# Performance work log

Hardware: AMD Instinct MI355X
Metric: run time of the kernel (lower is better)

The kernel has to match this reference:

```python
import jax, jax.numpy as jnp
import numpy as np

H = 96
W = 96
FX = 96.0
FY = 96.0
NEAR = 0.3
EPS = 1e-8


def q2r(quat):
    # quat: [N,4] (w,x,y,z) -> [N,3,3]
    q = quat / (jnp.linalg.norm(quat, axis=-1, keepdims=True) + 1e-12)
    w, x, y, z = q[:, 0], q[:, 1], q[:, 2], q[:, 3]
    R = jnp.stack([
        1 - 2 * (y * y + z * z), 2 * (x * y - w * z), 2 * (x * z + w * y),
        2 * (x * y + w * z), 1 - 2 * (x * x + z * z), 2 * (y * z - w * x),
        2 * (x * z - w * y), 2 * (y * z + w * x), 1 - 2 * (x * x + y * y),
    ], axis=-1).reshape(-1, 3, 3)
    return R


def setup_inputs() -> dict:
    key = jax.random.key(0)
    ks = jax.random.split(key, 8)
    N = 4096
    pos_xy = jax.random.uniform(ks[0], (N, 2), minval=-2.0, maxval=2.0, dtype=jnp.float32)
    pos_z = jax.random.uniform(ks[1], (N, 1), minval=2.0, maxval=6.0, dtype=jnp.float32)
    pos = jnp.concatenate([pos_xy, pos_z], axis=-1)
    rgb = jax.random.normal(ks[2], (N, 3), dtype=jnp.float32)
    opa = jax.random.normal(ks[3], (N,), dtype=jnp.float32)
    quat = jax.random.normal(ks[4], (N, 4), dtype=jnp.float32)
    scale = jax.random.uniform(ks[5], (N, 3), dtype=jnp.float32) * 0.05 + 0.005
    rot = jnp.eye(3, dtype=jnp.float32)
    tran = jnp.zeros(3, dtype=jnp.float32)
    return {"pos": pos, "rgb": rgb, "opa": opa, "quat": quat, "scale": scale, "rot": rot, "tran": tran}


def reference(pos, rgb, opa, quat, scale, rot, tran):
    # ---- project: world -> camera -> image space ----
    cam = pos @ rot.T + tran[None, :]              # [N,3]
    x, y, z = cam[:, 0], cam[:, 1], cam[:, 2]
    r = jnp.linalg.norm(cam, axis=-1)              # depth = ray length (camera_to_image)
    mean2d = jnp.stack([x / z, y / z], axis=-1)    # [N,2]

    # jacobian of (x/z, y/z, |p|) wrt camera-space point, [N,3,3]
    zeros = jnp.zeros_like(z)
    J = jnp.stack([
        1.0 / z, zeros, -x / (z * z),
        zeros, 1.0 / z, -y / (z * z),
        x / r, y / r, z / r,
    ], axis=-1).reshape(-1, 3, 3)

    # ---- 3D covariance: R S S^T R^T ----
    R = q2r(quat)                                   # [N,3,3]
    s = jnp.abs(scale) + 1e-4                       # [N,3]
    RS = R * s[:, None, :]                          # R @ diag(s)
    cov3d = jnp.einsum('nij,nkj->nik', RS, RS)      # [N,3,3]

    # ---- 2D covariance: (J W) cov3d (J W)^T, upper-left 2x2 ----
    JW = jnp.einsum('nij,jk->nik', J, rot)          # [N,3,3]
    cov2d = jnp.einsum('nij,njk,nlk->nil', JW, cov3d, JW)[:, :2, :2]  # [N,2,2]

    a = cov2d[:, 0, 0] + EPS
    d = cov2d[:, 1, 1] + EPS
    b = 0.5 * (cov2d[:, 0, 1] + cov2d[:, 1, 0])
    det = a * d - b * b
    inv_a = d / det
    inv_b = -b / det
    inv_d = a / det

    rgb_act = jax.nn.sigmoid(rgb)                   # [N,3]
    opa_act = jax.nn.sigmoid(opa)                   # [N]

    # ---- per-pixel gaussian evaluation in normalized image space ----
    u = (jnp.arange(W, dtype=jnp.float32) + 0.5 - W / 2) / FX   # [W]
    v = (jnp.arange(H, dtype=jnp.float32) + 0.5 - H / 2) / FY   # [H]
    pu = jnp.tile(u, H)                                          # [P]
    pv = jnp.repeat(v, W)                                        # [P]

    dx = pu[None, :] - mean2d[:, 0:1]               # [N,P]
    dy = pv[None, :] - mean2d[:, 1:2]               # [N,P]
    power = -0.5 * (inv_a[:, None] * dx * dx + 2.0 * inv_b[:, None] * dx * dy + inv_d[:, None] * dy * dy)
    alpha = opa_act[:, None] * jnp.exp(power)       # [N,P]
    alpha = jnp.clip(alpha, 0.0, 0.99)
    valid = (z > NEAR).astype(alpha.dtype)[:, None]
    alpha = alpha * valid

    # ---- depth-sorted alpha compositing ----
    order = jnp.argsort(r)                          # near -> far
    alpha_s = alpha[order]                          # [N,P]
    rgb_s = rgb_act[order]                          # [N,3]

    log_1m = jnp.log1p(-alpha_s)                    # [N,P]
    cum = jnp.cumsum(log_1m, axis=0)
    logT = jnp.concatenate([jnp.zeros((1, alpha_s.shape[1]), alpha_s.dtype), cum[:-1]], axis=0)
    w = jnp.exp(logT) * alpha_s                     # [N,P] blending weights
    img = jnp.einsum('np,nc->pc', w, rgb_s)         # [P,3]
    return img.reshape(H, W, 3)
```

## Files before the change

kernel.cpp:

```cpp
#include <hip/hip_runtime.h>
#include <math.h>

#define N_G   4096
#define IMW   96
#define TILE  6
#define TILES_X 16
#define NTILE (TILES_X*TILES_X)
#define NTHR  1024
#define NW    (NTHR/64)
#define NST   (N_G/NTHR)
#define NPX   (TILE*TILE)
#define NSEG  16
#define BCAP  2048
#define CAP   512
#define FXI   (1.0f/96.0f)
#define NEARP 0.3f
#define EPSV  1e-8f
#define LOG2E 1.4426950408889634f
#define LN2   0.6931471805599453f
#define CULL_K 26.0f

typedef unsigned long long ull;
typedef __attribute__((ext_vector_type(2))) unsigned long long ull2;

__global__ __launch_bounds__(NTHR, 1) void splat_k(
    const float* __restrict__ pos, const float* __restrict__ rgb,
    const float* __restrict__ opa, const float* __restrict__ quat,
    const float* __restrict__ scale, const float* __restrict__ rot,
    const float* __restrict__ tran, float* __restrict__ out)
{
    __shared__ unsigned int bl[BCAP];
    __shared__ __align__(16) ull skey[CAP+2];
    __shared__ int sslot[CAP];
    __shared__ float4 g0[CAP], g1[CAP];
    __shared__ float  g2[CAP];
    __shared__ float4 pix[NSEG*NPX];
    __shared__ int psum[4][CAP];
    __shared__ int bcnt_sh, cnt_sh;

    const int t = threadIdx.x;
    const int tile = blockIdx.x;
    const int tx = tile % TILES_X, ty = tile / TILES_X;
    const float u0 = ((float)(tx*TILE) + 0.5f - 48.0f) * FXI;
    const float u1 = u0 + (TILE-1) * FXI;
    const float v0 = ((float)(ty*TILE) + 0.5f - 48.0f) * FXI;
    const float v1 = v0 + (TILE-1) * FXI;
    const int wid = t >> 6, lane = t & 63;

    if (t == 0) { bcnt_sh = 0; cnt_sh = 0; }

    float R00=rot[0],R01=rot[1],R02=rot[2];
    float R10=rot[3],R11=rot[4],R12=rot[5];
    float R20=rot[6],R21=rot[7],R22=rot[8];
    float t0=tran[0], t1=tran[1], t2=tran[2];

    float pp0[NST], pp1[NST], pp2[NST], po[NST], ps0[NST], ps1[NST], ps2[NST];
    #pragma unroll
    for (int st = 0; st < NST; st++) {
        int gi = st*NTHR + t;
        pp0[st]=pos[gi*3+0]; pp1[st]=pos[gi*3+1]; pp2[st]=pos[gi*3+2];
        po[st]=opa[gi];
        ps0[st]=scale[gi*3+0]; ps1[st]=scale[gi*3+1]; ps2[st]=scale[gi*3+2];
    }
    __syncthreads();

    #pragma unroll
    for (int st = 0; st < NST; st++) {
        int gi = st*NTHR + t;
        float x = R00*pp0[st] + R01*pp1[st] + R02*pp2[st] + t0;
        float y = R10*pp0[st] + R11*pp1[st] + R12*pp2[st] + t1;
        float z = R20*pp0[st] + R21*pp1[st] + R22*pp2[st] + t2;
        float invz = 1.0f/z;
        float mu = x*invz, mv = y*invz;

        float inz2 = invz*invz;
        float fn = 2.0f*inz2 + (x*x + y*y)*inz2*inz2;
        float smax = fmaxf(fmaxf(fabsf(ps0[st]), fabsf(ps1[st])), fabsf(ps2[st])) + 1e-4f;
        float lmax = fn*smax*smax + EPSV;
        float amp = CULL_K + 1.0f + fminf(0.0f, po[st]*LOG2E);
        float r2b = amp * lmax * (2.0f*LN2) * 1.02f;

        float cu = fminf(fmaxf(mu, u0), u1);
        float cv = fminf(fmaxf(mv, v0), v1);
        float ddx = mu - cu, ddy = mv - cv;
        bool flag = (z > NEARP) && (amp > 0.0f) && (ddx*ddx + ddy*ddy <= r2b);

        ull m = __ballot(flag);
        int nm = __popcll(m);
        int base = 0;
        if (lane == 0 && nm) base = atomicAdd(&bcnt_sh, nm);
        base = __shfl(base, 0);
        if (flag) {
            int p = base + __popcll(m & ((1ull << lane) - 1ull));
            if (p < BCAP) bl[p] = (unsigned int)gi;
        }
    }
    __syncthreads();
    int bcnt = bcnt_sh; if (bcnt > BCAP) bcnt = BCAP;

    for (int s0i = 0; s0i < bcnt; s0i += NTHR) {
        int s = s0i + t;
        bool flag = false;
        float4 o0, o1; float ocb = 0.0f, rr = 0.0f;
        unsigned int gi = 0;
        if (s < bcnt) {
            gi = bl[s];
            float p0=pos[gi*3+0], p1=pos[gi*3+1], p2=pos[gi*3+2];
            float x = R00*p0 + R01*p1 + R02*p2 + t0;
            float y = R10*p0 + R11*p1 + R12*p2 + t1;
            float z = R20*p0 + R21*p1 + R22*p2 + t2;
            rr = sqrtf(x*x + y*y + z*z);
            float invz = 1.0f/z;
            float mu = x*invz, mv = y*invz;

            float J02 = -x*invz*invz, J12 = -y*invz*invz;
            float JW00 = invz*R00 + J02*R20;
            float JW01 = invz*R01 + J02*R21;
            float JW02 = invz*R02 + J02*R22;
            float JW10 = invz*R10 + J12*R20;
            float JW11 = invz*R11 + J12*R21;
            float JW12 = invz*R12 + J12*R22;

            float qw=quat[gi*4+0], qx=quat[gi*4+1], qy=quat[gi*4+2], qz=quat[gi*4+3];
            float qn = sqrtf(qw*qw+qx*qx+qy*qy+qz*qz) + 1e-12f;
            float qi = 1.0f/qn;
            qw*=qi; qx*=qi; qy*=qi; qz*=qi;
            float Q00=1.f-2.f*(qy*qy+qz*qz), Q01=2.f*(qx*qy-qw*qz), Q02=2.f*(qx*qz+qw*qy);
            float Q10=2.f*(qx*qy+qw*qz), Q11=1.f-2.f*(qx*qx+qz*qz), Q12=2.f*(qy*qz-qw*qx);
            float Q20=2.f*(qx*qz-qw*qy), Q21=2.f*(qy*qz+qw*qx), Q22=1.f-2.f*(qx*qx+qy*qy);

            float sa=fabsf(scale[gi*3+0])+1e-4f;
            float sb=fabsf(scale[gi*3+1])+1e-4f;
            float sc=fabsf(scale[gi*3+2])+1e-4f;
            float A00=Q00*sa,A01=Q01*sb,A02=Q02*sc;
            float A10=Q10*sa,A11=Q11*sb,A12=Q12*sc;
            float A20=Q20*sa,A21=Q21*sb,A22=Q22*sc;
            float C00=A00*A00+A01*A01+A02*A02;
            float C01=A00*A10+A01*A11+A02*A12;
            float C02=A00*A20+A01*A21+A02*A22;
            float C11=A10*A10+A11*A11+A12*A12;
            float C12=A10*A20+A11*A21+A12*A22;
            float C22=A20*A20+A21*A21+A22*A22;
            float M00=JW00*C00+JW01*C01+JW02*C02;
            float M01=JW00*C01+JW01*C11+JW02*C12;
            float M02=JW00*C02+JW01*C12+JW02*C22;
            float M10=JW10*C00+JW11*C01+JW12*C02;
            float M11=JW10*C01+JW11*C11+JW12*C12;
            float M12=JW10*C02+JW11*C12+JW12*C22;
            float a  = M00*JW00+M01*JW01+M02*JW02 + EPSV;
            float d  = M10*JW10+M11*JW11+M12*JW12 + EPSV;
            float bb = 0.5f*((M00*JW10+M01*JW11+M02*JW12)+(M10*JW00+M11*JW01+M12*JW02));
            float invdet = 1.0f/(a*d - bb*bb);
            float iaP = -0.5f*d*invdet*LOG2E;
            float ibP =  bb*invdet*LOG2E;
            float idP = -0.5f*a*invdet*LOG2E;

            float sig_o = 1.0f/(1.0f+__expf(-opa[gi]));
            float opa_eff = (z > NEARP) ? sig_o : 0.0f;

            float q00 = -iaP, q01 = -0.5f*ibP, q11 = -idP;
            float detQ = q00*q11 - q01*q01;
            float K = CULL_K + log2f(opa_eff);

            float cu = fminf(fmaxf(mu, u0), u1);
            float cv = fminf(fmaxf(mv, v0), v1);
            float ddx = mu - cu, ddy = mv - cv;
            flag = (ddx*ddx*detQ <= K*q11) && (ddy*ddy*detQ <= K*q00);

            if (flag) {
                float c0 = 1.0f/(1.0f+__expf(-rgb[gi*3+0]));
                float c1 = 1.0f/(1.0f+__expf(-rgb[gi*3+1]));
                float c2 = 1.0f/(1.0f+__expf(-rgb[gi*3+2]));
                o0 = make_float4(mu, mv, iaP, ibP);
                o1 = make_float4(idP, opa_eff, c0, c1);
                ocb = c2;
            }
        }
        ull m = __ballot(flag);
        int nm = __popcll(m);
        int base = 0;
        if (lane == 0 && nm) base = atomicAdd(&cnt_sh, nm);
        base = __shfl(base, 0);
        if (flag) {
            int p = base + __popcll(m & ((1ull << lane) - 1ull));
            if (p < CAP) {
                g0[p] = o0; g1[p] = o1; g2[p] = ocb;
                skey[p] = ((ull)__float_as_uint(rr) << 32) | gi;
            }
        }
    }
    __syncthreads();
    int cnt = cnt_sh; if (cnt > CAP) cnt = CAP;

    if (t == 0 && (cnt & 1)) skey[cnt] = ~0ull;
    __syncthreads();
    int cnt2 = cnt + (cnt & 1);
    int nq = cnt2 >> 1;
    const ull2* sk2 = (const ull2*)skey;
    const int g = t >> 8, e = t & 255;
    const bool h1 = (e < cnt), h2 = (e + 256 < cnt);
    ull kv1 = 0, kv2 = 0;
    if (h1) {
        kv1 = skey[e];
        if (h2) kv2 = skey[e + 256];
        int wA = (nq * g) >> 2;
        int wB = (nq * (g+1)) >> 2;
        int c1 = 0, c2 = 0;
        for (int w = wA; w < wB; w++) {
            ull2 p = sk2[w];
            c1 += (p.x < kv1) ? 1 : 0;
            c1 += (p.y < kv1) ? 1 : 0;
            c2 += (p.x < kv2) ? 1 : 0;
            c2 += (p.y < kv2) ? 1 : 0;
        }
        psum[g][e] = c1;
        if (h2) psum[g][e + 256] = c2;
    }
    __syncthreads();
    if (t < 256 && h1) {
        int r1 = psum[0][e] + psum[1][e] + psum[2][e] + psum[3][e];
        skey[r1]  = kv1;
        sslot[r1] = e;
        if (h2) {
            int e2 = e + 256;
            int r2 = psum[0][e2] + psum[1][e2] + psum[2][e2] + psum[3][e2];
            skey[r2]  = kv2;
            sslot[r2] = e2;
        }
    }
    __syncthreads();

    {
        const int seg = wid;
        const bool act = (lane < NPX);
        const int pid = act ? lane : 0;
        const int px = tx*TILE + (pid % TILE);
        const int py = ty*TILE + (pid / TILE);
        const float pu = ((float)px + 0.5f - 48.0f) * FXI;
        const float pv = ((float)py + 0.5f - 48.0f) * FXI;

        const int per = (cnt + NSEG - 1) / NSEG;
        const int sA = min(seg * per, cnt);
        const int sB = min(sA + per, cnt);

        float T = 1.0f, cr = 0.0f, cg = 0.0f, cb = 0.0f;
        for (int s = sA; s < sB; s++) {
            int slot = sslot[s];
            float4 a0 = g0[slot];
            float4 a1 = g1[slot];
            float  a2 = g2[slot];
            float dx = pu - a0.x;
            float dy = pv - a0.y;
            float pw = dx*(a0.z*dx + a0.w*dy) + a1.x*dy*dy;
            float al = fminf(a1.y * __builtin_amdgcn_exp2f(pw), 0.99f);
            float w = T * al;
            cr += w * a1.z;
            cg += w * a1.w;
            cb += w * a2;
            T *= (1.0f - al);
        }
        if (act) pix[seg*NPX + pid] = make_float4(cr, cg, cb, T);
    }
    __syncthreads();

    if (t < NPX) {
        float orr = 0.0f, og = 0.0f, ob = 0.0f, T2 = 1.0f;
        #pragma unroll
        for (int s = 0; s < NSEG; s++) {
            float4 P = pix[s*NPX + t];
            orr += T2 * P.x;
            og  += T2 * P.y;
            ob  += T2 * P.z;
            T2  *= P.w;
        }
        int px = tx*TILE + (t % TILE);
        int py = ty*TILE + (t / TILE);
        int pixel = py * IMW + px;
        out[pixel*3+0] = orr;
        out[pixel*3+1] = og;
        out[pixel*3+2] = ob;
    }
}

extern "C" void kernel_launch(void* const* d_in, const int* in_sizes, int n_in,
                              void* d_out, int out_size, void* d_ws, size_t ws_size,
                              hipStream_t stream) {
    const float* pos   = (const float*)d_in[0];
    const float* rgb   = (const float*)d_in[1];
    const float* opa   = (const float*)d_in[2];
    const float* quat  = (const float*)d_in[3];
    const float* scale = (const float*)d_in[4];
    const float* rot   = (const float*)d_in[5];
    const float* tran  = (const float*)d_in[6];
    float* out = (float*)d_out;

    splat_k<<<NTILE, NTHR, 0, stream>>>(pos, rgb, opa, quat, scale, rot, tran, out);
}
```

Baseline: 14.02 us.

## Split per-Gaussian preprocessing into a separate kernel shared by all tiles

Per-Gaussian projection, 2D covariance, inverse, activations and the elliptical cull extents are now computed once in a small prep kernel and written to workspace. The render kernel then does a single cull pass per tile against those precomputed extents and gathers the packed attributes. Before, every one of the 256 tiles recomputed the coarse cull for all 4096 Gaussians and the full covariance for the survivors. The cost is an extra kernel launch and global-memory round trips through the workspace, plus an exact ellipse-extent test that replaces the two-stage cull.

```diff
diff --git a/kernel.cpp b/kernel.cpp
--- a/kernel.cpp
+++ b/kernel.cpp
@@ -8,35 +8,116 @@
 #define NTILE (TILES_X*TILES_X)
 #define NTHR  1024
 #define NW    (NTHR/64)
-#define NST   (N_G/NTHR)
 #define NPX   (TILE*TILE)
 #define NSEG  16
-#define BCAP  2048
 #define CAP   512
 #define FXI   (1.0f/96.0f)
 #define NEARP 0.3f
 #define EPSV  1e-8f
 #define LOG2E 1.4426950408889634f
-#define LN2   0.6931471805599453f
 #define CULL_K 26.0f
 
 typedef unsigned long long ull;
 typedef __attribute__((ext_vector_type(2))) unsigned long long ull2;
 
-__global__ __launch_bounds__(NTHR, 1) void splat_k(
+__global__ __launch_bounds__(128) void prep_k(
     const float* __restrict__ pos, const float* __restrict__ rgb,
     const float* __restrict__ opa, const float* __restrict__ quat,
     const float* __restrict__ scale, const float* __restrict__ rot,
-    const float* __restrict__ tran, float* __restrict__ out)
+    const float* __restrict__ tran,
+    float4* __restrict__ cull, float4* __restrict__ p0a,
+    float4* __restrict__ p1a, float2* __restrict__ p2a)
 {
-    __shared__ unsigned int bl[BCAP];
+    int i = blockIdx.x * blockDim.x + threadIdx.x;
+    if (i >= N_G) return;
+
+    float R00=rot[0],R01=rot[1],R02=rot[2];
+    float R10=rot[3],R11=rot[4],R12=rot[5];
+    float R20=rot[6],R21=rot[7],R22=rot[8];
+    float t0=tran[0], t1=tran[1], t2=tran[2];
+
+    float p0 = pos[i*3+0], p1 = pos[i*3+1], p2 = pos[i*3+2];
+    float x = R00*p0 + R01*p1 + R02*p2 + t0;
+    float y = R10*p0 + R11*p1 + R12*p2 + t1;
+    float z = R20*p0 + R21*p1 + R22*p2 + t2;
+    float rr = sqrtf(x*x + y*y + z*z);
+    float invz = 1.0f/z;
+    float mu = x*invz, mv = y*invz;
+
+    float J02 = -x*invz*invz, J12 = -y*invz*invz;
+    float JW00 = invz*R00 + J02*R20;
+    float JW01 = invz*R01 + J02*R21;
+    float JW02 = invz*R02 + J02*R22;
+    float JW10 = invz*R10 + J12*R20;
+    float JW11 = invz*R11 + J12*R21;
+    float JW12 = invz*R12 + J12*R22;
+
+    float qw=quat[i*4+0], qx=quat[i*4+1], qy=quat[i*4+2], qz=quat[i*4+3];
+    float qn = sqrtf(qw*qw+qx*qx+qy*qy+qz*qz) + 1e-12f;
+    float qi = 1.0f/qn;
+    qw*=qi; qx*=qi; qy*=qi; qz*=qi;
+    float Q00=1.f-2.f*(qy*qy+qz*qz), Q01=2.f*(qx*qy-qw*qz), Q02=2.f*(qx*qz+qw*qy);
+    float Q10=2.f*(qx*qy+qw*qz), Q11=1.f-2.f*(qx*qx+qz*qz), Q12=2.f*(qy*qz-qw*qx);
+    float Q20=2.f*(qx*qz-qw*qy), Q21=2.f*(qy*qz+qw*qx), Q22=1.f-2.f*(qx*qx+qy*qy);
+
+    float sa=fabsf(scale[i*3+0])+1e-4f;
+    float sb=fabsf(scale[i*3+1])+1e-4f;
+    float sc=fabsf(scale[i*3+2])+1e-4f;
+    float A00=Q00*sa,A01=Q01*sb,A02=Q02*sc;
+    float A10=Q10*sa,A11=Q11*sb,A12=Q12*sc;
+    float A20=Q20*sa,A21=Q21*sb,A22=Q22*sc;
+    float C00=A00*A00+A01*A01+A02*A02;
+    float C01=A00*A10+A01*A11+A02*A12;
+    float C02=A00*A20+A01*A21+A02*A22;
+    float C11=A10*A10+A11*A11+A12*A12;
+    float C12=A10*A20+A11*A21+A12*A22;
+    float C22=A20*A20+A21*A21+A22*A22;
+    float M00=JW00*C00+JW01*C01+JW02*C02;
+    float M01=JW00*C01+JW01*C11+JW02*C12;
+    float M02=JW00*C02+JW01*C12+JW02*C22;
+    float M10=JW10*C00+JW11*C01+JW12*C02;
+    float M11=JW10*C01+JW11*C11+JW12*C12;
+    float M12=JW10*C02+JW11*C12+JW12*C22;
+    float a  = M00*JW00+M01*JW01+M02*JW02 + EPSV;
+    float d  = M10*JW10+M11*JW11+M12*JW12 + EPSV;
+    float bb = 0.5f*((M00*JW10+M01*JW11+M02*JW12)+(M10*JW00+M11*JW01+M12*JW02));
+    float invdet = 1.0f/(a*d - bb*bb);
+    float iaP = -0.5f*d*invdet*LOG2E;
+    float ibP =  bb*invdet*LOG2E;
+    float idP = -0.5f*a*invdet*LOG2E;
+
+    float sig_o = 1.0f/(1.0f+__expf(-opa[i]));
+    float opa_eff = (z > NEARP) ? sig_o : 0.0f;
+    float c0 = 1.0f/(1.0f+__expf(-rgb[i*3+0]));
+    float c1 = 1.0f/(1.0f+__expf(-rgb[i*3+1]));
+    float c2 = 1.0f/(1.0f+__expf(-rgb[i*3+2]));
+
+    float q00 = -iaP, q01 = -0.5f*ibP, q11 = -idP;
+    float detQ = q00*q11 - q01*q01;
+    float K = CULL_K + log2f(opa_eff);
+    float eu2, ev2;
+    if (detQ > 0.0f && K > 0.0f)      { eu2 = K*q11/detQ; ev2 = K*q00/detQ; }
+    else if (K > 0.0f)                { eu2 = 1e30f; ev2 = 1e30f; }
+    else                              { eu2 = -1.0f; ev2 = -1.0f; }
+
+    cull[i] = make_float4(mu, mv, eu2, ev2);
+    p0a[i]  = make_float4(mu, mv, iaP, ibP);
+    p1a[i]  = make_float4(idP, opa_eff, c0, c1);
+    p2a[i]  = make_float2(c2, rr);
+}
+
+__global__ __launch_bounds__(NTHR, 1) void render_k(
+    const float4* __restrict__ cull, const float4* __restrict__ p0a,
+    const float4* __restrict__ p1a, const float2* __restrict__ p2a,
+    float* __restrict__ out)
+{
     __shared__ __align__(16) ull skey[CAP+2];
     __shared__ int sslot[CAP];
     __shared__ float4 g0[CAP], g1[CAP];
     __shared__ float  g2[CAP];
     __shared__ float4 pix[NSEG*NPX];
     __shared__ int psum[4][CAP];
-    __shared__ int bcnt_sh, cnt_sh;
+    __shared__ int cnt_sh;
 
     const int t = threadIdx.x;
     const int tile = blockIdx.x;
@@ -47,135 +128,18 @@
     const float v1 = v0 + (TILE-1) * FXI;
     const int wid = t >> 6, lane = t & 63;
 
-    if (t == 0) { bcnt_sh = 0; cnt_sh = 0; }
-
-    float R00=rot[0],R01=rot[1],R02=rot[2];
-    float R10=rot[3],R11=rot[4],R12=rot[5];
-    float R20=rot[6],R21=rot[7],R22=rot[8];
-    float t0=tran[0], t1=tran[1], t2=tran[2];
-
-    float pp0[NST], pp1[NST], pp2[NST], po[NST], ps0[NST], ps1[NST], ps2[NST];
+    if (t == 0) cnt_sh = 0;
+    __syncthreads();
+
     #pragma unroll
-    for (int st = 0; st < NST; st++) {
-        int gi = st*NTHR + t;
-        pp0[st]=pos[gi*3+0]; pp1[st]=pos[gi*3+1]; pp2[st]=pos[gi*3+2];
-        po[st]=opa[gi];
-        ps0[st]=scale[gi*3+0]; ps1[st]=scale[gi*3+1]; ps2[st]=scale[gi*3+2];
-    }
-    __syncthreads();
-
-    #pragma unroll
-    for (int st = 0; st < NST; st++) {
-        int gi = st*NTHR + t;
-        float x = R00*pp0[st] + R01*pp1[st] + R02*pp2[st] + t0;
-        float y = R10*pp0[st] + R11*pp1[st] + R12*pp2[st] + t1;
-        float z = R20*pp0[st] + R21*pp1[st] + R22*pp2[st] + t2;
-        float invz = 1.0f/z;
-        float mu = x*invz, mv = y*invz;
-
-        float inz2 = invz*invz;
-        float fn = 2.0f*inz2 + (x*x + y*y)*inz2*inz2;
-        float smax = fmaxf(fmaxf(fabsf(ps0[st]), fabsf(ps1[st])), fabsf(ps2[st])) + 1e-4f;
-        float lmax = fn*smax*smax + EPSV;
-        float amp = CULL_K + 1.0f + fminf(0.0f, po[st]*LOG2E);
-        float r2b = amp * lmax * (2.0f*LN2) * 1.02f;
-
-        float cu = fminf(fmaxf(mu, u0), u1);
-        float cv = fminf(fmaxf(mv, v0), v1);
-        float ddx = mu - cu, ddy = mv - cv;
-        bool flag = (z > NEARP) && (amp > 0.0f) && (ddx*ddx + ddy*ddy <= r2b);
-
-        ull m = __ballot(flag);
-        int nm = __popcll(m);
-        int base = 0;
-        if (lane == 0 && nm) base = atomicAdd(&bcnt_sh, nm);
-        base = __shfl(base, 0);
-        if (flag) {
-            int p = base + __popcll(m & ((1ull << lane) - 1ull));
-            if (p < BCAP) bl[p] = (unsigned int)gi;
-        }
-    }
-    __syncthreads();
-    int bcnt = bcnt_sh; if (bcnt > BCAP) bcnt = BCAP;
-
-    for (int s0i = 0; s0i < bcnt; s0i += NTHR) {
-        int s = s0i + t;
-        bool flag = false;
-        float4 o0, o1; float ocb = 0.0f, rr = 0.0f;
-        unsigned int gi = 0;
-        if (s < bcnt) {
-            gi = bl[s];
-            float p0=pos[gi*3+0], p1=pos[gi*3+1], p2=pos[gi*3+2];
-            float x = R00*p0 + R01*p1 + R02*p2 + t0;
-            float y = R10*p0 + R11*p1 + R12*p2 + t1;
-            float z = R20*p0 + R21*p1 + R22*p2 + t2;
-            rr = sqrtf(x*x + y*y + z*z);
-            float invz = 1.0f/z;
-            float mu = x*invz, mv = y*invz;
-
-            float J02 = -x*invz*invz, J12 = -y*invz*invz;
-            float JW00 = invz*R00 + J02*R20;
-            float JW01 = invz*R01 + J02*R21;
-            float JW02 = invz*R02 + J02*R22;
-            float JW10 = invz*R10 + J12*R20;
-            float JW11 = invz*R11 + J12*R21;
-            float JW12 = invz*R12 + J12*R22;
-
-            float qw=quat[gi*4+0], qx=quat[gi*4+1], qy=quat[gi*4+2], qz=quat[gi*4+3];
-            float qn = sqrtf(qw*qw+qx*qx+qy*qy+qz*qz) + 1e-12f;
-            float qi = 1.0f/qn;
-            qw*=qi; qx*=qi; qy*=qi; qz*=qi;
-            float Q00=1.f-2.f*(qy*qy+qz*qz), Q01=2.f*(qx*qy-qw*qz), Q02=2.f*(qx*qz+qw*qy);
-            float Q10=2.f*(qx*qy+qw*qz), Q11=1.f-2.f*(qx*qx+qz*qz), Q12=2.f*(qy*qz-qw*qx);
-            float Q20=2.f*(qx*qz-qw*qy), Q21=2.f*(qy*qz+qw*qx), Q22=1.f-2.f*(qx*qx+qy*qy);
-
-            float sa=fabsf(scale[gi*3+0])+1e-4f;
-            float sb=fabsf(scale[gi*3+1])+1e-4f;
-            float sc=fabsf(scale[gi*3+2])+1e-4f;
-            float A00=Q00*sa,A01=Q01*sb,A02=Q02*sc;
-            float A10=Q10*sa,A11=Q11*sb,A12=Q12*sc;
-            float A20=Q20*sa,A21=Q21*sb,A22=Q22*sc;
-            float C00=A00*A00+A01*A01+A02*A02;
-            float C01=A00*A10+A01*A11+A02*A12;
-            float C02=A00*A20+A01*A21+A02*A22;
-            float C11=A10*A10+A11*A11+A12*A12;
-            float C12=A10*A20+A11*A21+A12*A22;
-            float C22=A20*A20+A21*A21+A22*A22;
-            float M00=JW00*C00+JW01*C01+JW02*C02;
-            float M01=JW00*C01+JW01*C11+JW02*C12;
-            float M02=JW00*C02+JW01*C12+JW02*C22;
-            float M10=JW10*C00+JW11*C01+JW12*C02;
-            float M11=JW10*C01+JW11*C11+JW12*C12;
-            float M12=JW10*C02+JW11*C12+JW12*C22;
-            float a  = M00*JW00+M01*JW01+M02*JW02 + EPSV;
-            float d  = M10*JW10+M11*JW11+M12*JW12 + EPSV;
-            float bb = 0.5f*((M00*JW10+M01*JW11+M02*JW12)+(M10*JW00+M11*JW01+M12*JW02));
-            float invdet = 1.0f/(a*d - bb*bb);
-            float iaP = -0.5f*d*invdet*LOG2E;
-            float ibP =  bb*invdet*LOG2E;
-            float idP = -0.5f*a*invdet*LOG2E;
-
-            float sig_o = 1.0f/(1.0f+__expf(-opa[gi]));
-            float opa_eff = (z > NEARP) ? sig_o : 0.0f;
-
-            float q00 = -iaP, q01 = -0.5f*ibP, q11 = -idP;
-            float detQ = q00*q11 - q01*q01;
-            float K = CULL_K + log2f(opa_eff);
-
-            float cu = fminf(fmaxf(mu, u0), u1);
-            float cv = fminf(fmaxf(mv, v0), v1);
-            float ddx = mu - cu, ddy = mv - cv;
-            flag = (ddx*ddx*detQ <= K*q11) && (ddy*ddy*detQ <= K*q00);
-
-            if (flag) {
-                float c0 = 1.0f/(1.0f+__expf(-rgb[gi*3+0]));
-                float c1 = 1.0f/(1.0f+__expf(-rgb[gi*3+1]));
-                float c2 = 1.0f/(1.0f+__expf(-rgb[gi*3+2]));
-                o0 = make_float4(mu, mv, iaP, ibP);
-                o1 = make_float4(idP, opa_eff, c0, c1);
-                ocb = c2;
-            }
-        }
+    for (int k = 0; k < N_G/NTHR; k++) {
+        int gi = k*NTHR + t;
+        float4 cq = cull[gi];
+        float cu = fminf(fmaxf(cq.x, u0), u1);
+        float cv = fminf(fmaxf(cq.y, v0), v1);
+        float ddx = cq.x - cu, ddy = cq.y - cv;
+        bool flag = (ddx*ddx <= cq.z) && (ddy*ddy <= cq.w);
+
         ull m = __ballot(flag);
         int nm = __popcll(m);
         int base = 0;
@@ -184,8 +148,11 @@
         if (flag) {
             int p = base + __popcll(m & ((1ull << lane) - 1ull));
             if (p < CAP) {
-                g0[p] = o0; g1[p] = o1; g2[p] = ocb;
-                skey[p] = ((ull)__float_as_uint(rr) << 32) | gi;
+                float4 a0 = p0a[gi];
+                float4 a1 = p1a[gi];
+                float2 a2 = p2a[gi];
+                g0[p] = a0; g1[p] = a1; g2[p] = a2.x;
+                skey[p] = ((ull)__float_as_uint(a2.y) << 32) | (unsigned int)gi;
             }
         }
     }
@@ -294,5 +261,13 @@
     const float* tran  = (const float*)d_in[6];
     float* out = (float*)d_out;
 
-    splat_k<<<NTILE, NTHR, 0, stream>>>(pos, rgb, opa, quat, scale, rot, tran, out);
+    char* ws = (char*)d_ws;
+    float4* cull = (float4*)ws;
+    float4* p0a  = (float4*)(ws + 65536);
+    float4* p1a  = (float4*)(ws + 131072);
+    float2* p2a  = (float2*)(ws + 196608);
+
+    prep_k<<<N_G/128, 128, 0, stream>>>(pos, rgb, opa, quat, scale, rot, tran,
+                                        cull, p0a, p1a, p2a);
+    render_k<<<NTILE, NTHR, 0, stream>>>(cull, p0a, p1a, p2a, out);
 }
```

Result: slower. 17.18 us (+22.5%).

## Stage gaussian inputs in LDS with vector loads and tighten coarse cull

Applied to the files above, without the earlier changes.

Copies pos, scale and opa into shared memory using coalesced float4 loads, so both the coarse cull pass and the gathered refine pass read from LDS instead of making scattered global loads. The coarse cull test changes from a single radial bound to separate per-axis bounds, which is meant to pass fewer candidates to the expensive refine stage. The psum and pix scratch buffers now alias the staged position array to keep LDS usage within budget, and BCAP is reduced. This raises LDS footprint and adds aliasing hazards, and the smaller BCAP risks overflowing the candidate list.

```diff
diff --git a/kernel.cpp b/kernel.cpp
--- a/kernel.cpp
+++ b/kernel.cpp
@@ -11,7 +11,7 @@
 #define NST   (N_G/NTHR)
 #define NPX   (TILE*TILE)
 #define NSEG  16
-#define BCAP  2048
+#define BCAP  1536
 #define CAP   512
 #define FXI   (1.0f/96.0f)
 #define NEARP 0.3f
@@ -29,13 +29,14 @@
     const float* __restrict__ scale, const float* __restrict__ rot,
     const float* __restrict__ tran, float* __restrict__ out)
 {
+    __shared__ float spos[N_G*3];
+    __shared__ float sscale[N_G*3];
+    __shared__ float sopa[N_G];
     __shared__ unsigned int bl[BCAP];
     __shared__ __align__(16) ull skey[CAP+2];
     __shared__ int sslot[CAP];
     __shared__ float4 g0[CAP], g1[CAP];
     __shared__ float  g2[CAP];
-    __shared__ float4 pix[NSEG*NPX];
-    __shared__ int psum[4][CAP];
     __shared__ int bcnt_sh, cnt_sh;
 
     const int t = threadIdx.x;
@@ -47,43 +48,56 @@
     const float v1 = v0 + (TILE-1) * FXI;
     const int wid = t >> 6, lane = t & 63;
 
-    if (t == 0) { bcnt_sh = 0; cnt_sh = 0; }
-
     float R00=rot[0],R01=rot[1],R02=rot[2];
     float R10=rot[3],R11=rot[4],R12=rot[5];
     float R20=rot[6],R21=rot[7],R22=rot[8];
     float t0=tran[0], t1=tran[1], t2=tran[2];
 
-    float pp0[NST], pp1[NST], pp2[NST], po[NST], ps0[NST], ps1[NST], ps2[NST];
+    {
+        const float4* p4 = (const float4*)pos;
+        const float4* s4 = (const float4*)scale;
+        const float4* o4 = (const float4*)opa;
+        float4* sp4 = (float4*)spos;
+        float4* ss4 = (float4*)sscale;
+        float4* so4 = (float4*)sopa;
+        #pragma unroll
+        for (int k = 0; k < 3; k++) {
+            sp4[k*NTHR + t] = p4[k*NTHR + t];
+            ss4[k*NTHR + t] = s4[k*NTHR + t];
+        }
+        so4[t] = o4[t];
+    }
+    if (t == 0) { bcnt_sh = 0; cnt_sh = 0; }
+    __syncthreads();
+
     #pragma unroll
     for (int st = 0; st < NST; st++) {
         int gi = st*NTHR + t;
-        pp0[st]=pos[gi*3+0]; pp1[st]=pos[gi*3+1]; pp2[st]=pos[gi*3+2];
-        po[st]=opa[gi];
-        ps0[st]=scale[gi*3+0]; ps1[st]=scale[gi*3+1]; ps2[st]=scale[gi*3+2];
-    }
-    __syncthreads();
-
-    #pragma unroll
-    for (int st = 0; st < NST; st++) {
-        int gi = st*NTHR + t;
-        float x = R00*pp0[st] + R01*pp1[st] + R02*pp2[st] + t0;
-        float y = R10*pp0[st] + R11*pp1[st] + R12*pp2[st] + t1;
-        float z = R20*pp0[st] + R21*pp1[st] + R22*pp2[st] + t2;
+        float p0 = spos[gi*3+0], p1 = spos[gi*3+1], p2 = spos[gi*3+2];
+        float o  = sopa[gi];
+        float s0 = sscale[gi*3+0], s1 = sscale[gi*3+1], s2v = sscale[gi*3+2];
+
+        float x = R00*p0 + R01*p1 + R02*p2 + t0;
+        float y = R10*p0 + R11*p1 + R12*p2 + t1;
+        float z = R20*p0 + R21*p1 + R22*p2 + t2;
         float invz = 1.0f/z;
         float mu = x*invz, mv = y*invz;
 
         float inz2 = invz*invz;
-        float fn = 2.0f*inz2 + (x*x + y*y)*inz2*inz2;
-        float smax = fmaxf(fmaxf(fabsf(ps0[st]), fabsf(ps1[st])), fabsf(ps2[st])) + 1e-4f;
-        float lmax = fn*smax*smax + EPSV;
-        float amp = CULL_K + 1.0f + fminf(0.0f, po[st]*LOG2E);
-        float r2b = amp * lmax * (2.0f*LN2) * 1.02f;
+        float fnu = inz2 + x*x*inz2*inz2;
+        float fnv = inz2 + y*y*inz2*inz2;
+        float smax = fmaxf(fmaxf(fabsf(s0), fabsf(s1)), fabsf(s2v)) + 1e-4f;
+        float s2 = smax*smax;
+        float amp = CULL_K + 1.0f + fminf(0.0f, o*LOG2E);
+        float sc2 = amp * (2.0f*LN2) * 1.02f;
+        float eu2b = sc2 * (fnu*s2 + EPSV);
+        float ev2b = sc2 * (fnv*s2 + EPSV);
 
         float cu = fminf(fmaxf(mu, u0), u1);
         float cv = fminf(fmaxf(mv, v0), v1);
         float ddx = mu - cu, ddy = mv - cv;
-        bool flag = (z > NEARP) && (amp > 0.0f) && (ddx*ddx + ddy*ddy <= r2b);
+        bool flag = (z > NEARP) && (amp > 0.0f) &&
+                    (ddx*ddx <= eu2b) && (ddy*ddy <= ev2b);
 
         ull m = __ballot(flag);
         int nm = __popcll(m);
@@ -105,7 +119,7 @@
         unsigned int gi = 0;
         if (s < bcnt) {
             gi = bl[s];
-            float p0=pos[gi*3+0], p1=pos[gi*3+1], p2=pos[gi*3+2];
+            float p0 = spos[gi*3+0], p1 = spos[gi*3+1], p2 = spos[gi*3+2];
             float x = R00*p0 + R01*p1 + R02*p2 + t0;
             float y = R10*p0 + R11*p1 + R12*p2 + t1;
             float z = R20*p0 + R21*p1 + R22*p2 + t2;
@@ -121,7 +135,8 @@
             float JW11 = invz*R11 + J12*R21;
             float JW12 = invz*R12 + J12*R22;
 
-            float qw=quat[gi*4+0], qx=quat[gi*4+1], qy=quat[gi*4+2], qz=quat[gi*4+3];
+            const float4 qv = ((const float4*)quat)[gi];
+            float qw=qv.x, qx=qv.y, qy=qv.z, qz=qv.w;
             float qn = sqrtf(qw*qw+qx*qx+qy*qy+qz*qz) + 1e-12f;
             float qi = 1.0f/qn;
             qw*=qi; qx*=qi; qy*=qi; qz*=qi;
@@ -129,9 +144,9 @@
             float Q10=2.f*(qx*qy+qw*qz), Q11=1.f-2.f*(qx*qx+qz*qz), Q12=2.f*(qy*qz-qw*qx);
             float Q20=2.f*(qx*qz-qw*qy), Q21=2.f*(qy*qz+qw*qx), Q22=1.f-2.f*(qx*qx+qy*qy);
 
-            float sa=fabsf(scale[gi*3+0])+1e-4f;
-            float sb=fabsf(scale[gi*3+1])+1e-4f;
-            float sc=fabsf(scale[gi*3+2])+1e-4f;
+            float sa=fabsf(sscale[gi*3+0])+1e-4f;
+            float sb=fabsf(sscale[gi*3+1])+1e-4f;
+            float sc=fabsf(sscale[gi*3+2])+1e-4f;
             float A00=Q00*sa,A01=Q01*sb,A02=Q02*sc;
             float A10=Q10*sa,A11=Q11*sb,A12=Q12*sc;
             float A20=Q20*sa,A21=Q21*sb,A22=Q22*sc;
@@ -155,7 +170,7 @@
             float ibP =  bb*invdet*LOG2E;
             float idP = -0.5f*a*invdet*LOG2E;
 
-            float sig_o = 1.0f/(1.0f+__expf(-opa[gi]));
+            float sig_o = 1.0f/(1.0f+__expf(-sopa[gi]));
             float opa_eff = (z > NEARP) ? sig_o : 0.0f;
 
             float q00 = -iaP, q01 = -0.5f*ibP, q11 = -idP;
@@ -191,6 +206,9 @@
     }
     __syncthreads();
     int cnt = cnt_sh; if (cnt > CAP) cnt = CAP;
+
+    int (*psum)[CAP] = (int (*)[CAP])(void*)spos;
+    float4* pix = (float4*)(void*)(spos + 2048);
 
     if (t == 0 && (cnt & 1)) skey[cnt] = ~0ull;
     __syncthreads();
```

New measurement: 14.13 us. About the same (+0.8%).
